# Optimization experiments

Hardware: AMD Instinct MI355X
Metric: run time of the kernel (lower is better)

Reference implementation:

```python
import jax, jax.numpy as jnp
import numpy as np

EPS = 1e-12  # matches torch.nn.functional.normalize default eps


def setup_inputs() -> dict:
    key = jax.random.key(0)
    k1, k2 = jax.random.split(key)
    x = jax.random.normal(k1, (2, 32, 64, 128, 128), dtype=jnp.float32)
    gamma = jax.random.normal(k2, (1,), dtype=jnp.float32)
    return {"x": x, "gamma": gamma}


def reference(x, gamma):
    B, N, C, H, W = x.shape
    D = C * H * W
    q = x.reshape(B, N, D)  # proj_query == proj_value == flattened x
    # F.normalize(q, dim=-1): L2 norm per row, clamped to eps.
    # Key is q^T normalized along dim=-2, i.e. same row-normalized q.
    norm = jnp.sqrt(jnp.sum(q * q, axis=-1, keepdims=True))
    qn = q / jnp.maximum(norm, EPS)
    # energy: [B, N, N] cosine-similarity matrix
    energy = jnp.einsum('bnd,bmd->bnm', qn, qn)
    # max-subtract trick (note: max - energy, inverted attention)
    energy_new = jnp.max(energy, axis=-1, keepdims=True) - energy
    attention = jax.nn.softmax(energy_new, axis=-1)
    out = jnp.einsum('bnm,bmd->bnd', attention, q)
    out = out.reshape(B, N, C, H, W)
    out = gamma * out + x
    return out.reshape(B, N * C, H, W)
```

## Files before the change

kernel.cpp:

```cpp
#include <hip/hip_runtime.h>


#define NROW 32
static const size_t D_FULL = 1048576ull;
#define EPSN 1e-12f

typedef __attribute__((ext_vector_type(8)))  __bf16 bf16x8;
typedef __attribute__((ext_vector_type(4)))  __bf16 bf16x4;
typedef __attribute__((ext_vector_type(16))) float  f32x16;
typedef __attribute__((ext_vector_type(4)))  float  f32x4;

__global__ __launch_bounds__(256) void k_zero(float* g) {
    int i = blockIdx.x * 256 + threadIdx.x;
    ((float4*)g)[i] = make_float4(0.f, 0.f, 0.f, 0.f);
}

#define GSTRIDE 520
__global__ __launch_bounds__(256, 4) void k_gram(const float* __restrict__ x,
                                                 float* __restrict__ gpart) {
    __shared__ __align__(16) unsigned char smem[NROW * GSTRIDE * 2];
    __bf16* tile = (__bf16*)smem;
    float (*red)[1024] = (float (*)[1024])smem;

    const int tid  = threadIdx.x;
    const int w    = tid >> 6;
    const int lane = tid & 63;
    const int b    = (int)(blockIdx.x >> 9);
    const size_t dblk = ((size_t)(blockIdx.x & 511)) * 2048;
    const int row  = lane & 31;
    const int kg   = lane >> 5;

    const float* xb = x + (size_t)b * NROW * D_FULL + dblk;
    const int srow0 = tid >> 7;
    const int sc4   = tid & 127;

    f32x16 acc = (f32x16)(0.0f);

    for (int s = 0; s < 4; ++s) {
        __syncthreads();
        const float* src = xb + s * 512;
        #pragma unroll
        for (int sw = 0; sw < 16; ++sw) {
            int r = sw * 2 + srow0;
            float4 v = *(const float4*)(src + (size_t)r * D_FULL + sc4 * 4);
            bf16x4 h;
            h[0] = (__bf16)v.x; h[1] = (__bf16)v.y;
            h[2] = (__bf16)v.z; h[3] = (__bf16)v.w;
            *(bf16x4*)&tile[r * GSTRIDE + sc4 * 4] = h;
        }
        __syncthreads();
        #pragma unroll
        for (int kk = 0; kk < 8; ++kk) {
            int kstep = w * 8 + kk;
            bf16x8 f = *(const bf16x8*)&tile[row * GSTRIDE + kstep * 16 + kg * 8];
            acc = __builtin_amdgcn_mfma_f32_32x32x16_bf16(f, f, acc, 0, 0, 0);
        }
    }
    __syncthreads();

    const int col  = lane & 31;
    const int rsel = lane >> 5;
    #pragma unroll
    for (int r = 0; r < 16; ++r) {
        int rw = (r & 3) + 8 * (r >> 2) + 4 * rsel;
        red[w][rw * 32 + col] = acc[r];
    }
    __syncthreads();

    float* dst = gpart + (size_t)(blockIdx.x & 7) * 2048 + (size_t)b * 1024;
    for (int e = tid; e < 1024; e += 256) {
        float sum = red[0][e] + red[1][e] + red[2][e] + red[3][e];
        atomicAdd(&dst[e], sum);
    }
}

__global__ __launch_bounds__(1024) void k_attn(const float* __restrict__ gpart,
                                               const float* __restrict__ gamma_p,
                                               float* __restrict__ M) {
    const int b   = blockIdx.x;
    const int tid = threadIdx.x;
    const int n   = tid >> 5;
    const int m   = tid & 31;

    float g = 0.f;
    #pragma unroll
    for (int s = 0; s < 8; ++s) g += gpart[(size_t)s * 2048 + (size_t)b * 1024 + tid];

    __shared__ float nrm[32];
    if (n == m) nrm[n] = fmaxf(sqrtf(g), EPSN);
    __syncthreads();

    float e = g / (nrm[n] * nrm[m]);

    float rmin = e;
    #pragma unroll
    for (int off = 16; off > 0; off >>= 1) rmin = fminf(rmin, __shfl_xor(rmin, off, 32));
    float pv  = expf(rmin - e);
    float sum = pv;
    #pragma unroll
    for (int off = 16; off > 0; off >>= 1) sum += __shfl_xor(sum, off, 32);
    float a = pv / sum;

    M[(size_t)b * 1024 + tid] = gamma_p[0] * a + (n == m ? 1.f : 0.f);
}

__device__ __forceinline__ void fma4(float4& o, float c, const float4& a) {
    o.x += c * a.x; o.y += c * a.y; o.z += c * a.z; o.w += c * a.w;
}

__global__ __launch_bounds__(256) void k_apply(const float* __restrict__ x,
                                               const float* __restrict__ M,
                                               float* __restrict__ out) {
    __shared__ __align__(16) float Ml[1024];
    const int tid = threadIdx.x;
    const int b   = blockIdx.x >> 10;
    const float* Mb = M + (size_t)b * 1024;
    #pragma unroll
    for (int i = 0; i < 4; ++i) Ml[tid + i * 256] = Mb[tid + i * 256];
    __syncthreads();

    const size_t d4  = ((size_t)(blockIdx.x & 1023)) * 256 + tid;
    const size_t rs4 = D_FULL / 4;
    const float4* xb = (const float4*)(x) + (size_t)b * NROW * rs4;
    f32x4*        ob = (f32x4*)(out)      + (size_t)b * NROW * rs4;

    float4 qv[32];
    #pragma unroll
    for (int m = 0; m < 32; ++m) qv[m] = xb[(size_t)m * rs4 + d4];

    for (int n = 0; n < 32; ++n) {
        const float4* Mr = (const float4*)(&Ml[n * 32]);
        float4 o = make_float4(0.f, 0.f, 0.f, 0.f);
        #pragma unroll
        for (int m4 = 0; m4 < 8; ++m4) {
            float4 c = Mr[m4];
            fma4(o, c.x, qv[m4 * 4 + 0]);
            fma4(o, c.y, qv[m4 * 4 + 1]);
            fma4(o, c.z, qv[m4 * 4 + 2]);
            fma4(o, c.w, qv[m4 * 4 + 3]);
        }
        f32x4 ov; ov[0] = o.x; ov[1] = o.y; ov[2] = o.z; ov[3] = o.w;
        __builtin_nontemporal_store(ov, &ob[(size_t)n * rs4 + d4]);
    }
}

extern "C" void kernel_launch(void* const* d_in, const int* in_sizes, int n_in,
                              void* d_out, int out_size, void* d_ws, size_t ws_size,
                              hipStream_t stream) {
    const float* x     = (const float*)d_in[0];
    const float* gamma = (const float*)d_in[1];
    float*       out   = (float*)d_out;
    float*       ws    = (float*)d_ws;

    float* gpart = ws;
    float* Mws   = ws + 16384;

    k_zero <<<16,   256,  0, stream>>>(gpart);
    k_gram <<<1024, 256,  0, stream>>>(x, gpart);
    k_attn <<<2,    1024, 0, stream>>>(gpart, gamma, Mws);
    k_apply<<<2048, 256,  0, stream>>>(x, Mws, out);
}
```

Measured before the change: 524.3 us.

## Prefetch next gram stage into registers and stream apply loads in chunks

Measured after the change: 567.5 us. 8.2% more time.

```diff
diff --git a/kernel.cpp b/kernel.cpp
--- a/kernel.cpp
+++ b/kernel.cpp
@@ -35,20 +35,34 @@
     const int sc4   = tid & 127;
 
     f32x16 acc = (f32x16)(0.0f);
+    float4 vreg[16];
+
+    #pragma unroll
+    for (int sw = 0; sw < 16; ++sw) {
+        int r = sw * 2 + srow0;
+        vreg[sw] = *(const float4*)(xb + (size_t)r * D_FULL + sc4 * 4);
+    }
 
     for (int s = 0; s < 4; ++s) {
         __syncthreads();
-        const float* src = xb + s * 512;
         #pragma unroll
         for (int sw = 0; sw < 16; ++sw) {
             int r = sw * 2 + srow0;
-            float4 v = *(const float4*)(src + (size_t)r * D_FULL + sc4 * 4);
+            float4 v = vreg[sw];
             bf16x4 h;
             h[0] = (__bf16)v.x; h[1] = (__bf16)v.y;
             h[2] = (__bf16)v.z; h[3] = (__bf16)v.w;
             *(bf16x4*)&tile[r * GSTRIDE + sc4 * 4] = h;
         }
         __syncthreads();
+        if (s < 3) {
+            const float* src = xb + (s + 1) * 512;
+            #pragma unroll
+            for (int sw = 0; sw < 16; ++sw) {
+                int r = sw * 2 + srow0;
+                vreg[sw] = *(const float4*)(src + (size_t)r * D_FULL + sc4 * 4);
+            }
+        }
         #pragma unroll
         for (int kk = 0; kk < 8; ++kk) {
             int kstep = w * 8 + kk;
@@ -108,9 +122,20 @@
     o.x += c * a.x; o.y += c * a.y; o.z += c * a.z; o.w += c * a.w;
 }
 
-__global__ __launch_bounds__(256) void k_apply(const float* __restrict__ x,
-                                               const float* __restrict__ M,
-                                               float* __restrict__ out) {
+#define ACC8(Q, MB)                                               \
+    _Pragma("unroll")                                             \
+    for (int n = 0; n < 32; ++n) {                                \
+        const float4 c0 = *(const float4*)&Ml[n * 32 + (MB)];     \
+        const float4 c1 = *(const float4*)&Ml[n * 32 + (MB) + 4]; \
+        fma4(o[n], c0.x, Q[0]); fma4(o[n], c0.y, Q[1]);           \
+        fma4(o[n], c0.z, Q[2]); fma4(o[n], c0.w, Q[3]);           \
+        fma4(o[n], c1.x, Q[4]); fma4(o[n], c1.y, Q[5]);           \
+        fma4(o[n], c1.z, Q[6]); fma4(o[n], c1.w, Q[7]);           \
+    }
+
+__global__ __launch_bounds__(256, 2) void k_apply(const float* __restrict__ x,
+                                                  const float* __restrict__ M,
+                                                  float* __restrict__ out) {
     __shared__ __align__(16) float Ml[1024];
     const int tid = threadIdx.x;
     const int b   = blockIdx.x >> 10;
@@ -124,22 +149,27 @@
     const float4* xb = (const float4*)(x) + (size_t)b * NROW * rs4;
     f32x4*        ob = (f32x4*)(out)      + (size_t)b * NROW * rs4;
 
-    float4 qv[32];
+    float4 o[32];
     #pragma unroll
-    for (int m = 0; m < 32; ++m) qv[m] = xb[(size_t)m * rs4 + d4];
+    for (int n = 0; n < 32; ++n) o[n] = make_float4(0.f, 0.f, 0.f, 0.f);
 
+    float4 qa[8], qb[8];
+    #pragma unroll
+    for (int m = 0; m < 8; ++m) qa[m] = xb[(size_t)m * rs4 + d4];
+    #pragma unroll
+    for (int m = 0; m < 8; ++m) qb[m] = xb[(size_t)(8 + m) * rs4 + d4];
+    ACC8(qa, 0)
+    #pragma unroll
+    for (int m = 0; m < 8; ++m) qa[m] = xb[(size_t)(16 + m) * rs4 + d4];
+    ACC8(qb, 8)
+    #pragma unroll
+    for (int m = 0; m < 8; ++m) qb[m] = xb[(size_t)(24 + m) * rs4 + d4];
+    ACC8(qa, 16)
+    ACC8(qb, 24)
+
+    #pragma unroll
     for (int n = 0; n < 32; ++n) {
-        const float4* Mr = (const float4*)(&Ml[n * 32]);
-        float4 o = make_float4(0.f, 0.f, 0.f, 0.f);
-        #pragma unroll
-        for (int m4 = 0; m4 < 8; ++m4) {
-            float4 c = Mr[m4];
-            fma4(o, c.x, qv[m4 * 4 + 0]);
-            fma4(o, c.y, qv[m4 * 4 + 1]);
-            fma4(o, c.z, qv[m4 * 4 + 2]);
-            fma4(o, c.w, qv[m4 * 4 + 3]);
-        }
-        f32x4 ov; ov[0] = o.x; ov[1] = o.y; ov[2] = o.z; ov[3] = o.w;
+        f32x4 ov; ov[0] = o[n].x; ov[1] = o[n].y; ov[2] = o[n].z; ov[3] = o[n].w;
         __builtin_nontemporal_store(ov, &ob[(size_t)n * rs4 + d4]);
     }
 }
```
